# Optimization experiments

Hardware: AMD Instinct MI355X
Metric: run time of the kernel (lower is better)

## Reference

```python
import jax, jax.numpy as jnp
import numpy as np

N_NODES = 50000


def _gcn_conv(x, W, b, src, dst, n_nodes):
    """PyG GCNConv: add self-loops, symmetric normalization, aggregate, linear, bias.
    x: [N, Fin], W: [Fin, Fout], b: [Fout], src/dst: [E] int.
    """
    loop = jnp.arange(n_nodes, dtype=src.dtype)
    src_f = jnp.concatenate([src, loop])  # [E + N]
    dst_f = jnp.concatenate([dst, loop])
    # degree over incoming edges (edge weights are all 1 after self-loops)
    deg = jax.ops.segment_sum(jnp.ones_like(src_f, dtype=x.dtype), dst_f,
                              num_segments=n_nodes)
    dinv = jnp.where(deg > 0, jax.lax.rsqrt(deg), 0.0)
    norm = dinv[src_f] * dinv[dst_f]  # [E + N]
    h = x @ W  # [N, Fout] -- transform before propagate (Fin >= Fout path)
    msg = h[src_f] * norm[:, None]  # gather + per-edge scale
    out = jax.ops.segment_sum(msg, dst_f, num_segments=n_nodes)  # scatter-add
    return out + b


def setup_inputs() -> dict:
    key = jax.random.key(0)
    k_x, k_e, k_w1, k_w2 = jax.random.split(key, 4)
    in_ch, out_ch = 128, 64
    hid = 2 * out_ch
    n_edges = 800000
    x = jax.random.normal(k_x, (N_NODES, in_ch), dtype=jnp.float32)
    edge_index = jax.random.randint(k_e, (2, n_edges), 0, N_NODES, dtype=jnp.int64)
    # Glorot-ish init for weights, zero bias (matches PyG defaults)
    W1 = jax.random.normal(k_w1, (in_ch, hid), dtype=jnp.float32) / np.sqrt(in_ch)
    b1 = jnp.zeros((hid,), dtype=jnp.float32)
    W2 = jax.random.normal(k_w2, (hid, out_ch), dtype=jnp.float32) / np.sqrt(hid)
    b2 = jnp.zeros((out_ch,), dtype=jnp.float32)
    return {"x": x, "edge_index": edge_index, "W1": W1, "b1": b1, "W2": W2, "b2": b2}


def reference(x, edge_index, W1, b1, W2, b2):
    src, dst = edge_index[0], edge_index[1]
    h = jnp.tanh(_gcn_conv(x, W1, b1, src, dst, N_NODES))
    return _gcn_conv(h, W2, b2, src, dst, N_NODES)
```

## Files before the change

kernel.cpp:

```cpp
#include <hip/hip_runtime.h>
#include <stdint.h>

#define N_NODES 50000
#define IN_CH   128
#define HID     128
#define OUT_CH  64

#define CBITS 8
#define NCB   ((N_NODES + 255) >> 8)
#define CAP   8192
#define APB   4096

#define XPAD  136

typedef unsigned int   uint32;
typedef unsigned short ushort16;
typedef __attribute__((ext_vector_type(8))) short short8;
typedef __attribute__((ext_vector_type(4))) float f32x4;

static __device__ __forceinline__ ushort16 f32_to_bf16(float f) {
    uint32 u = __float_as_uint(f);
    u = (u + 0x7fffu + ((u >> 16) & 1u)) >> 16;
    return (ushort16)u;
}
static __device__ __forceinline__ float bf16lo_to_f32(uint32 u) {
    return __uint_as_float(u << 16);
}
static __device__ __forceinline__ float bf16hi_to_f32(uint32 u) {
    return __uint_as_float(u & 0xffff0000u);
}


__global__ __launch_bounds__(256) void passA_kernel(
    const int* __restrict__ src, const int* __restrict__ dst,
    int* __restrict__ gcur, uint32* __restrict__ ebuf2, int E) {
    __shared__ int hist[256];
    __shared__ int excl[256];
    __shared__ int fcur[256];
    __shared__ int gbase[256];
    __shared__ uint32 obuf[APB];
    const int t = threadIdx.x;
    const int e0 = blockIdx.x * APB;
    const int nv = min(APB, E - e0);

    hist[t] = 0;
    __syncthreads();

    uint32 u[16];
    #pragma unroll
    for (int j = 0; j < 16; ++j) {
        int i = t + 256 * j;
        u[j] = 0xffffffffu;
        if (i < nv) {
            int e = e0 + i;
            int s = src[e], d = dst[e];
            if ((unsigned)d < N_NODES && (unsigned)s < N_NODES) {
                u[j] = (uint32)s | ((uint32)d << 16);
                atomicAdd(&hist[(unsigned)d >> CBITS], 1);
            }
        }
    }
    __syncthreads();

    excl[t] = hist[t];
    __syncthreads();
    #pragma unroll
    for (int off = 1; off < 256; off <<= 1) {
        int v = (t >= off) ? excl[t - off] : 0;
        __syncthreads();
        excl[t] += v;
        __syncthreads();
    }
    int myexcl = excl[t] - hist[t];
    if (hist[t] > 0) gbase[t] = t * CAP + atomicAdd(&gcur[t], hist[t]);
    __syncthreads();
    excl[t] = myexcl;
    fcur[t] = myexcl;
    __syncthreads();

    #pragma unroll
    for (int j = 0; j < 16; ++j) {
        if (u[j] != 0xffffffffu) {
            int b = u[j] >> (16 + CBITS);
            int pos = atomicAdd(&fcur[b], 1);
            obuf[pos] = u[j];
        }
    }
    __syncthreads();

    for (int i = t; i < nv; i += 256) {
        uint32 v = obuf[i];
        int b = v >> (16 + CBITS);
        int gpos = gbase[b] + (i - excl[b]);
        if (gpos < (b + 1) * CAP) ebuf2[gpos] = v;
    }
}

__global__ __launch_bounds__(256) void interlude_kernel(
    const int* __restrict__ gcur, int* __restrict__ ecnt, int* __restrict__ eoff) {
    __shared__ int sd[256];
    int t = threadIdx.x;
    int c = (t < NCB) ? gcur[t] : 0;
    sd[t] = c;
    __syncthreads();
    #pragma unroll
    for (int off = 1; off < 256; off <<= 1) {
        int v = (t >= off) ? sd[t - off] : 0;
        __syncthreads();
        sd[t] += v;
        __syncthreads();
    }
    if (t < NCB) { ecnt[t] = c; eoff[t] = sd[t] - c; }
}

__global__ __launch_bounds__(256) void passB_kernel(
    const uint32* __restrict__ ebuf2, const int* __restrict__ ecnt,
    const int* __restrict__ eoff, ushort16* __restrict__ ebuf16,
    int* __restrict__ offs, int* __restrict__ degi, float* __restrict__ dinv) {
    __shared__ uint32 sbuf[CAP];
    __shared__ ushort16 obuf[CAP];
    __shared__ int fh[256];
    __shared__ int fx[256];
    __shared__ int fc[256];
    const int b = blockIdx.x, t = threadIdx.x;
    const int nb = ecnt[b];
    const int base = b * CAP;
    const int obase = eoff[b];

    fh[t] = 0;
    __syncthreads();
    for (int i = t; i < nb; i += 256) {
        uint32 v = ebuf2[base + i];
        sbuf[i] = v;
        atomicAdd(&fh[(v >> 16) & 255], 1);
    }
    __syncthreads();

    fx[t] = fh[t];
    __syncthreads();
    #pragma unroll
    for (int off = 1; off < 256; off <<= 1) {
        int v = (t >= off) ? fx[t - off] : 0;
        __syncthreads();
        fx[t] += v;
        __syncthreads();
    }
    int ex = fx[t] - fh[t];
    fc[t] = ex;

    int n = b * 256 + t;
    if (n < N_NODES) {
        degi[n] = fh[t];
        offs[n] = obase + ex;
        dinv[n] = rsqrtf(1.0f + (float)fh[t]);
    }
    __syncthreads();

    for (int i = t; i < nb; i += 256) {
        uint32 v = sbuf[i];
        int nl = (v >> 16) & 255;
        int pos = atomicAdd(&fc[nl], 1);
        obuf[pos] = (ushort16)(v & 0xffffu);
    }
    __syncthreads();
    for (int i = t; i < nb; i += 256) ebuf16[obase + i] = obuf[i];
}

__global__ __launch_bounds__(256) void prep_w_kernel(
    const float* __restrict__ W1, const float* __restrict__ W2,
    ushort16* __restrict__ w1t, ushort16* __restrict__ w2t) {
    int i = blockIdx.x * 256 + threadIdx.x;
    if (i < 128 * 128) {
        int k = i >> 7, n = i & 127;
        w1t[n * 128 + k] = f32_to_bf16(W1[k * 128 + n]);
    }
    if (i < 128 * 64) {
        int k = i >> 6, n = i & 63;
        w2t[n * 128 + k] = f32_to_bf16(W2[k * 64 + n]);
    }
}

__global__ __launch_bounds__(256) void gemm1_mfma_kernel(
    const float* __restrict__ x, const ushort16* __restrict__ w1t,
    ushort16* __restrict__ h1b) {
    __shared__ __align__(16) ushort16 xs[64 * XPAD];
    __shared__ __align__(16) ushort16 wt[128 * XPAD];
    const int tid = threadIdx.x;
    const int block_row = blockIdx.x * 64;

    {
        const uint4* g = (const uint4*)w1t;
        #pragma unroll
        for (int j = 0; j < 8; ++j) {
            int idx = tid + 256 * j;
            int row = idx >> 4, c = idx & 15;
            uint4 v = g[idx];
            *(uint4*)&wt[row * XPAD + c * 8] = v;
        }
    }
    {
        #pragma unroll
        for (int j = 0; j < 8; ++j) {
            int idx = tid + 256 * j;
            int row = idx >> 5, c4 = idx & 31;
            int gr = block_row + row; if (gr >= N_NODES) gr = N_NODES - 1;
            float4 v = *(const float4*)(x + (size_t)gr * IN_CH + c4 * 4);
            uint32 p0 = (uint32)f32_to_bf16(v.x) | ((uint32)f32_to_bf16(v.y) << 16);
            uint32 p1 = (uint32)f32_to_bf16(v.z) | ((uint32)f32_to_bf16(v.w) << 16);
            uint32* dp = (uint32*)&xs[row * XPAD + c4 * 4];
            dp[0] = p0; dp[1] = p1;
        }
    }
    __syncthreads();

    const int wv = tid >> 6, lane = tid & 63;
    const int r16 = lane & 15, kq = lane >> 4;
    f32x4 acc[8];
    #pragma unroll
    for (int n = 0; n < 8; ++n) acc[n] = (f32x4){0.f, 0.f, 0.f, 0.f};

    const ushort16* xrow = &xs[(wv * 16 + r16) * XPAD + kq * 8];
    #pragma unroll
    for (int kk = 0; kk < 4; ++kk) {
        short8 a = *(const short8*)(xrow + kk * 32);
        #pragma unroll
        for (int n = 0; n < 8; ++n) {
            short8 b = *(const short8*)&wt[(n * 16 + r16) * XPAD + kk * 32 + kq * 8];
            acc[n] = __builtin_amdgcn_mfma_f32_16x16x32_bf16(a, b, acc[n], 0, 0, 0);
        }
    }

    #pragma unroll
    for (int n = 0; n < 8; ++n) {
        #pragma unroll
        for (int j = 0; j < 4; ++j) {
            int gr = block_row + wv * 16 + kq * 4 + j;
            if (gr < N_NODES)
                h1b[(size_t)gr * HID + n * 16 + r16] = f32_to_bf16(acc[n][j]);
        }
    }
}

__global__ __launch_bounds__(256) void gather1_kernel(
    const int* __restrict__ offs, const int* __restrict__ degi,
    const ushort16* __restrict__ ebuf16, const float* __restrict__ dinv,
    const ushort16* __restrict__ h1b, const float* __restrict__ b1,
    ushort16* __restrict__ a1b) {
    int node = blockIdx.x * 4 + (threadIdx.x >> 6);
    int lane = threadIdx.x & 63;
    if (node >= N_NODES) return;
    float di = dinv[node];
    int beg = offs[node];
    int cnt = degi[node];

    uint32 us = ((const uint32*)(h1b + (size_t)node * HID))[lane];
    float ax = bf16lo_to_f32(us) * di * di;
    float ay = bf16hi_to_f32(us) * di * di;

    for (int base = 0; base < cnt; base += 64) {
        int m = min(cnt - base, 64);
        int e_l = 0; float w_l = 0.f;
        if (lane < m) { e_l = ebuf16[beg + base + lane]; w_l = dinv[e_l] * di; }
        int i = 0;
        for (; i + 8 <= m; i += 8) {
            int s0 = __shfl(e_l, i),     s1 = __shfl(e_l, i + 1);
            int s2 = __shfl(e_l, i + 2), s3 = __shfl(e_l, i + 3);
            int s4 = __shfl(e_l, i + 4), s5 = __shfl(e_l, i + 5);
            int s6 = __shfl(e_l, i + 6), s7 = __shfl(e_l, i + 7);
            float w0 = __shfl(w_l, i),     w1 = __shfl(w_l, i + 1);
            float w2 = __shfl(w_l, i + 2), w3 = __shfl(w_l, i + 3);
            float w4 = __shfl(w_l, i + 4), w5 = __shfl(w_l, i + 5);
            float w6 = __shfl(w_l, i + 6), w7 = __shfl(w_l, i + 7);
            uint32 u0 = ((const uint32*)(h1b + (size_t)s0 * HID))[lane];
            uint32 u1 = ((const uint32*)(h1b + (size_t)s1 * HID))[lane];
            uint32 u2 = ((const uint32*)(h1b + (size_t)s2 * HID))[lane];
            uint32 u3 = ((const uint32*)(h1b + (size_t)s3 * HID))[lane];
            uint32 u4 = ((const uint32*)(h1b + (size_t)s4 * HID))[lane];
            uint32 u5 = ((const uint32*)(h1b + (size_t)s5 * HID))[lane];
            uint32 u6 = ((const uint32*)(h1b + (size_t)s6 * HID))[lane];
            uint32 u7 = ((const uint32*)(h1b + (size_t)s7 * HID))[lane];
            ax += bf16lo_to_f32(u0) * w0 + bf16lo_to_f32(u1) * w1
                + bf16lo_to_f32(u2) * w2 + bf16lo_to_f32(u3) * w3
                + bf16lo_to_f32(u4) * w4 + bf16lo_to_f32(u5) * w5
                + bf16lo_to_f32(u6) * w6 + bf16lo_to_f32(u7) * w7;
            ay += bf16hi_to_f32(u0) * w0 + bf16hi_to_f32(u1) * w1
                + bf16hi_to_f32(u2) * w2 + bf16hi_to_f32(u3) * w3
                + bf16hi_to_f32(u4) * w4 + bf16hi_to_f32(u5) * w5
                + bf16hi_to_f32(u6) * w6 + bf16hi_to_f32(u7) * w7;
        }
        for (; i + 2 <= m; i += 2) {
            int s0 = __shfl(e_l, i), s1 = __shfl(e_l, i + 1);
            float w0 = __shfl(w_l, i), w1 = __shfl(w_l, i + 1);
            uint32 u0 = ((const uint32*)(h1b + (size_t)s0 * HID))[lane];
            uint32 u1 = ((const uint32*)(h1b + (size_t)s1 * HID))[lane];
            ax += bf16lo_to_f32(u0) * w0 + bf16lo_to_f32(u1) * w1;
            ay += bf16hi_to_f32(u0) * w0 + bf16hi_to_f32(u1) * w1;
        }
        for (; i < m; ++i) {
            int s0 = __shfl(e_l, i);
            float w0 = __shfl(w_l, i);
            uint32 u0 = ((const uint32*)(h1b + (size_t)s0 * HID))[lane];
            ax += bf16lo_to_f32(u0) * w0;
            ay += bf16hi_to_f32(u0) * w0;
        }
    }
    float2 bb = ((const float2*)b1)[lane];
    float tx = tanhf(ax + bb.x);
    float ty = tanhf(ay + bb.y);
    uint32 pk = (uint32)f32_to_bf16(tx) | ((uint32)f32_to_bf16(ty) << 16);
    ((uint32*)(a1b + (size_t)node * HID))[lane] = pk;
}

__global__ __launch_bounds__(256) void gemm2_mfma_kernel(
    const ushort16* __restrict__ a1b, const ushort16* __restrict__ w2t,
    ushort16* __restrict__ h2b) {
    __shared__ __align__(16) ushort16 xs[64 * XPAD];
    __shared__ __align__(16) ushort16 wt[64 * XPAD];
    const int tid = threadIdx.x;
    const int block_row = blockIdx.x * 64;

    {
        const uint4* g = (const uint4*)w2t;
        #pragma unroll
        for (int j = 0; j < 4; ++j) {
            int idx = tid + 256 * j;
            int row = idx >> 4, c = idx & 15;
            uint4 v = g[idx];
            *(uint4*)&wt[row * XPAD + c * 8] = v;
        }
    }
    {
        #pragma unroll
        for (int j = 0; j < 4; ++j) {
            int idx = tid + 256 * j;
            int row = idx >> 4, c = idx & 15;
            int gr = block_row + row; if (gr >= N_NODES) gr = N_NODES - 1;
            uint4 v = *(const uint4*)(a1b + (size_t)gr * HID + c * 8);
            *(uint4*)&xs[row * XPAD + c * 8] = v;
        }
    }
    __syncthreads();

    const int wv = tid >> 6, lane = tid & 63;
    const int r16 = lane & 15, kq = lane >> 4;
    f32x4 acc[4];
    #pragma unroll
    for (int n = 0; n < 4; ++n) acc[n] = (f32x4){0.f, 0.f, 0.f, 0.f};

    const ushort16* xrow = &xs[(wv * 16 + r16) * XPAD + kq * 8];
    #pragma unroll
    for (int kk = 0; kk < 4; ++kk) {
        short8 a = *(const short8*)(xrow + kk * 32);
        #pragma unroll
        for (int n = 0; n < 4; ++n) {
            short8 b = *(const short8*)&wt[(n * 16 + r16) * XPAD + kk * 32 + kq * 8];
            acc[n] = __builtin_amdgcn_mfma_f32_16x16x32_bf16(a, b, acc[n], 0, 0, 0);
        }
    }

    #pragma unroll
    for (int n = 0; n < 4; ++n) {
        #pragma unroll
        for (int j = 0; j < 4; ++j) {
            int gr = block_row + wv * 16 + kq * 4 + j;
            if (gr < N_NODES)
                h2b[(size_t)gr * OUT_CH + n * 16 + r16] = f32_to_bf16(acc[n][j]);
        }
    }
}

__global__ __launch_bounds__(256) void gather2_kernel(
    const int* __restrict__ offs, const int* __restrict__ degi,
    const ushort16* __restrict__ ebuf16, const float* __restrict__ dinv,
    const ushort16* __restrict__ h2b, const float* __restrict__ b2,
    float* __restrict__ out) {
    int node = blockIdx.x * 4 + (threadIdx.x >> 6);
    int lane = threadIdx.x & 63;
    if (node >= N_NODES) return;
    float di = dinv[node];
    int beg = offs[node];
    int cnt = degi[node];

    float self = __uint_as_float(((uint32)h2b[(size_t)node * OUT_CH + lane]) << 16);
    float acc = b2[lane] + self * di * di;

    for (int base = 0; base < cnt; base += 64) {
        int m = min(cnt - base, 64);
        int e_l = 0; float w_l = 0.f;
        if (lane < m) { e_l = ebuf16[beg + base + lane]; w_l = dinv[e_l] * di; }
        int i = 0;
        for (; i + 8 <= m; i += 8) {
            int s0 = __shfl(e_l, i),     s1 = __shfl(e_l, i + 1);
            int s2 = __shfl(e_l, i + 2), s3 = __shfl(e_l, i + 3);
            int s4 = __shfl(e_l, i + 4), s5 = __shfl(e_l, i + 5);
            int s6 = __shfl(e_l, i + 6), s7 = __shfl(e_l, i + 7);
            float w0 = __shfl(w_l, i),     w1 = __shfl(w_l, i + 1);
            float w2 = __shfl(w_l, i + 2), w3 = __shfl(w_l, i + 3);
            float w4 = __shfl(w_l, i + 4), w5 = __shfl(w_l, i + 5);
            float w6 = __shfl(w_l, i + 6), w7 = __shfl(w_l, i + 7);
            float v0 = __uint_as_float(((uint32)h2b[(size_t)s0 * OUT_CH + lane]) << 16);
            float v1 = __uint_as_float(((uint32)h2b[(size_t)s1 * OUT_CH + lane]) << 16);
            float v2 = __uint_as_float(((uint32)h2b[(size_t)s2 * OUT_CH + lane]) << 16);
            float v3 = __uint_as_float(((uint32)h2b[(size_t)s3 * OUT_CH + lane]) << 16);
            float v4 = __uint_as_float(((uint32)h2b[(size_t)s4 * OUT_CH + lane]) << 16);
            float v5 = __uint_as_float(((uint32)h2b[(size_t)s5 * OUT_CH + lane]) << 16);
            float v6 = __uint_as_float(((uint32)h2b[(size_t)s6 * OUT_CH + lane]) << 16);
            float v7 = __uint_as_float(((uint32)h2b[(size_t)s7 * OUT_CH + lane]) << 16);
            acc += v0 * w0 + v1 * w1 + v2 * w2 + v3 * w3
                 + v4 * w4 + v5 * w5 + v6 * w6 + v7 * w7;
        }
        for (; i + 2 <= m; i += 2) {
            int s0 = __shfl(e_l, i), s1 = __shfl(e_l, i + 1);
            float w0 = __shfl(w_l, i), w1 = __shfl(w_l, i + 1);
            float v0 = __uint_as_float(((uint32)h2b[(size_t)s0 * OUT_CH + lane]) << 16);
            float v1 = __uint_as_float(((uint32)h2b[(size_t)s1 * OUT_CH + lane]) << 16);
            acc += v0 * w0 + v1 * w1;
        }
        for (; i < m; ++i) {
            int s0 = __shfl(e_l, i);
            float w0 = __shfl(w_l, i);
            float v0 = __uint_as_float(((uint32)h2b[(size_t)s0 * OUT_CH + lane]) << 16);
            acc += v0 * w0;
        }
    }
    out[(size_t)node * OUT_CH + lane] = acc;
}

extern "C" void kernel_launch(void* const* d_in, const int* in_sizes, int n_in,
                              void* d_out, int out_size, void* d_ws, size_t ws_size,
                              hipStream_t stream) {
    const float* x  = (const float*)d_in[0];
    const int*   ei = (const int*)d_in[1];
    const float* W1 = (const float*)d_in[2];
    const float* b1 = (const float*)d_in[3];
    const float* W2 = (const float*)d_in[4];
    const float* b2 = (const float*)d_in[5];
    float* out = (float*)d_out;

    const int E = in_sizes[1] / 2;
    const int* src = ei;
    const int* dst = ei + E;

    float* dinv   = (float*)d_ws;
    int* degi     = (int*)(dinv + N_NODES);
    int* offs     = degi + N_NODES;
    int* gcur     = offs + N_NODES;
    int* ecnt     = gcur + NCB;
    int* eoff     = ecnt + NCB;
    ushort16* w1t = (ushort16*)(eoff + NCB);
    ushort16* w2t = w1t + 128 * 128;
    ushort16* ebuf16 = w2t + 64 * 128;
    uintptr_t p   = (uintptr_t)(ebuf16 + E);
    p = (p + 15) & ~(uintptr_t)15;
    ushort16* a1b = (ushort16*)p;
    uint32* ebuf2 = (uint32*)a1b;
    ushort16* h1b = a1b + (size_t)N_NODES * HID;
    ushort16* h2b = h1b + (size_t)N_NODES * HID;

    hipMemsetAsync(gcur, 0, NCB * sizeof(int), stream);
    passA_kernel<<<(E + APB - 1) / APB, 256, 0, stream>>>(src, dst, gcur, ebuf2, E);
    interlude_kernel<<<1, 256, 0, stream>>>(gcur, ecnt, eoff);
    passB_kernel<<<NCB, 256, 0, stream>>>(ebuf2, ecnt, eoff, ebuf16, offs, degi, dinv);
    prep_w_kernel<<<64, 256, 0, stream>>>(W1, W2, w1t, w2t);

    gemm1_mfma_kernel<<<(N_NODES + 63) / 64, 256, 0, stream>>>(x, w1t, h1b);
    gather1_kernel<<<(N_NODES + 3) / 4, 256, 0, stream>>>(offs, degi, ebuf16, dinv, h1b, b1, a1b);
    gemm2_mfma_kernel<<<(N_NODES + 63) / 64, 256, 0, stream>>>(a1b, w2t, h2b);
    gather2_kernel<<<(N_NODES + 3) / 4, 256, 0, stream>>>(offs, degi, ebuf16, dinv, h2b, b2, out);
}
```

Measured before the change: 121.1 us.

## Merge preprocessing kernels and co-schedule GEMM1 with CSR build; use readlane in gathers

```diff
diff --git a/kernel.cpp b/kernel.cpp
--- a/kernel.cpp
+++ b/kernel.cpp
@@ -7,11 +7,12 @@
 #define OUT_CH  64
 
 #define CBITS 8
-#define NCB   ((N_NODES + 255) >> 8)
+#define NCB   196
 #define CAP   8192
 #define APB   4096
 
 #define XPAD  136
+#define G1BLK 782
 
 typedef unsigned int   uint32;
 typedef unsigned short ushort16;
@@ -29,17 +30,34 @@
 static __device__ __forceinline__ float bf16hi_to_f32(uint32 u) {
     return __uint_as_float(u & 0xffff0000u);
 }
-
-
-__global__ __launch_bounds__(256) void passA_kernel(
+#define RLI(v, l) __builtin_amdgcn_readlane((v), (l))
+#define RLF(v, l) __uint_as_float((uint32)__builtin_amdgcn_readlane((int)__float_as_uint(v), (l)))
+
+__global__ __launch_bounds__(256) void build1_kernel(
     const int* __restrict__ src, const int* __restrict__ dst,
-    int* __restrict__ gcur, uint32* __restrict__ ebuf2, int E) {
+    int* __restrict__ gcur, uint32* __restrict__ ebuf2, int E, int nA,
+    const float* __restrict__ W1, const float* __restrict__ W2,
+    ushort16* __restrict__ w1t, ushort16* __restrict__ w2t) {
     __shared__ int hist[256];
     __shared__ int excl[256];
     __shared__ int fcur[256];
     __shared__ int gbase[256];
     __shared__ uint32 obuf[APB];
     const int t = threadIdx.x;
+
+    if ((int)blockIdx.x >= nA) {
+        int i = ((int)blockIdx.x - nA) * 256 + t;
+        if (i < 128 * 128) {
+            int k = i >> 7, n = i & 127;
+            w1t[n * 128 + k] = f32_to_bf16(W1[k * 128 + n]);
+        }
+        if (i < 128 * 64) {
+            int k = i >> 6, n = i & 63;
+            w2t[n * 128 + k] = f32_to_bf16(W2[k * 64 + n]);
+        }
+        return;
+    }
+
     const int e0 = blockIdx.x * APB;
     const int nv = min(APB, E - e0);
 
@@ -96,41 +114,102 @@
     }
 }
 
-__global__ __launch_bounds__(256) void interlude_kernel(
-    const int* __restrict__ gcur, int* __restrict__ ecnt, int* __restrict__ eoff) {
-    __shared__ int sd[256];
-    int t = threadIdx.x;
-    int c = (t < NCB) ? gcur[t] : 0;
-    sd[t] = c;
-    __syncthreads();
-    #pragma unroll
-    for (int off = 1; off < 256; off <<= 1) {
-        int v = (t >= off) ? sd[t - off] : 0;
-        __syncthreads();
-        sd[t] += v;
-        __syncthreads();
-    }
-    if (t < NCB) { ecnt[t] = c; eoff[t] = sd[t] - c; }
-}
-
-__global__ __launch_bounds__(256) void passB_kernel(
-    const uint32* __restrict__ ebuf2, const int* __restrict__ ecnt,
-    const int* __restrict__ eoff, ushort16* __restrict__ ebuf16,
-    int* __restrict__ offs, int* __restrict__ degi, float* __restrict__ dinv) {
-    __shared__ uint32 sbuf[CAP];
-    __shared__ ushort16 obuf[CAP];
-    __shared__ int fh[256];
-    __shared__ int fx[256];
-    __shared__ int fc[256];
-    const int b = blockIdx.x, t = threadIdx.x;
-    const int nb = ecnt[b];
-    const int base = b * CAP;
-    const int obase = eoff[b];
+__global__ __launch_bounds__(256) void build2_kernel(
+    const uint32* __restrict__ ebuf2, const int* __restrict__ gcur,
+    ushort16* __restrict__ ebuf16, int* __restrict__ offs,
+    int* __restrict__ degi, float* __restrict__ dinv,
+    const float* __restrict__ x, const ushort16* __restrict__ w1t,
+    ushort16* __restrict__ h1b) {
+    __shared__ __align__(16) char smem[53248];
+    const int t = threadIdx.x;
+
+    if (blockIdx.x >= NCB) {
+        ushort16* xs = (ushort16*)smem;
+        ushort16* wt = (ushort16*)(smem + 64 * XPAD * 2);
+        const int block_row = ((int)blockIdx.x - NCB) * 64;
+
+        {
+            const uint4* g = (const uint4*)w1t;
+            #pragma unroll
+            for (int j = 0; j < 8; ++j) {
+                int idx = t + 256 * j;
+                int row = idx >> 4, c = idx & 15;
+                uint4 v = g[idx];
+                *(uint4*)&wt[row * XPAD + c * 8] = v;
+            }
+        }
+        {
+            #pragma unroll
+            for (int j = 0; j < 8; ++j) {
+                int idx = t + 256 * j;
+                int row = idx >> 5, c4 = idx & 31;
+                int gr = block_row + row; if (gr >= N_NODES) gr = N_NODES - 1;
+                float4 v = *(const float4*)(x + (size_t)gr * IN_CH + c4 * 4);
+                uint32 p0 = (uint32)f32_to_bf16(v.x) | ((uint32)f32_to_bf16(v.y) << 16);
+                uint32 p1 = (uint32)f32_to_bf16(v.z) | ((uint32)f32_to_bf16(v.w) << 16);
+                uint32* dp = (uint32*)&xs[row * XPAD + c4 * 4];
+                dp[0] = p0; dp[1] = p1;
+            }
+        }
+        __syncthreads();
+
+        const int wv = t >> 6, lane = t & 63;
+        const int r16 = lane & 15, kq = lane >> 4;
+        f32x4 acc[8];
+        #pragma unroll
+        for (int n = 0; n < 8; ++n) acc[n] = (f32x4){0.f, 0.f, 0.f, 0.f};
+
+        const ushort16* xrow = &xs[(wv * 16 + r16) * XPAD + kq * 8];
+        #pragma unroll
+        for (int kk = 0; kk < 4; ++kk) {
+            short8 a = *(const short8*)(xrow + kk * 32);
+            #pragma unroll
+            for (int n = 0; n < 8; ++n) {
+                short8 b = *(const short8*)&wt[(n * 16 + r16) * XPAD + kk * 32 + kq * 8];
+                acc[n] = __builtin_amdgcn_mfma_f32_16x16x32_bf16(a, b, acc[n], 0, 0, 0);
+            }
+        }
+
+        #pragma unroll
+        for (int n = 0; n < 8; ++n) {
+            #pragma unroll
+            for (int j = 0; j < 4; ++j) {
+                int gr = block_row + wv * 16 + kq * 4 + j;
+                if (gr < N_NODES)
+                    h1b[(size_t)gr * HID + n * 16 + r16] = f32_to_bf16(acc[n][j]);
+            }
+        }
+        return;
+    }
+
+    uint32*   sbuf = (uint32*)smem;
+    ushort16* obuf = (ushort16*)(smem + CAP * 4);
+    int* fh = (int*)(smem + CAP * 4 + CAP * 2);
+    int* fx = fh + 256;
+    int* fc = fx + 256;
+    int* gs = fc + 256;
+    const int b = blockIdx.x;
+
+    {
+        int c = (t < NCB) ? min(gcur[t], CAP) : 0;
+        gs[t] = c;
+        __syncthreads();
+        #pragma unroll
+        for (int off = 1; off < 256; off <<= 1) {
+            int v = (t >= off) ? gs[t - off] : 0;
+            __syncthreads();
+            gs[t] += v;
+            __syncthreads();
+        }
+    }
+    const int nb = min(gcur[b], CAP);
+    const int obase = gs[b] - nb;
+    __syncthreads();
 
     fh[t] = 0;
     __syncthreads();
     for (int i = t; i < nb; i += 256) {
-        uint32 v = ebuf2[base + i];
+        uint32 v = ebuf2[b * CAP + i];
         sbuf[i] = v;
         atomicAdd(&fh[(v >> 16) & 255], 1);
     }
@@ -164,81 +243,6 @@
     }
     __syncthreads();
     for (int i = t; i < nb; i += 256) ebuf16[obase + i] = obuf[i];
-}
-
-__global__ __launch_bounds__(256) void prep_w_kernel(
-    const float* __restrict__ W1, const float* __restrict__ W2,
-    ushort16* __restrict__ w1t, ushort16* __restrict__ w2t) {
-    int i = blockIdx.x * 256 + threadIdx.x;
-    if (i < 128 * 128) {
-        int k = i >> 7, n = i & 127;
-        w1t[n * 128 + k] = f32_to_bf16(W1[k * 128 + n]);
-    }
-    if (i < 128 * 64) {
-        int k = i >> 6, n = i & 63;
-        w2t[n * 128 + k] = f32_to_bf16(W2[k * 64 + n]);
-    }
-}
-
-__global__ __launch_bounds__(256) void gemm1_mfma_kernel(
-    const float* __restrict__ x, const ushort16* __restrict__ w1t,
-    ushort16* __restrict__ h1b) {
-    __shared__ __align__(16) ushort16 xs[64 * XPAD];
-    __shared__ __align__(16) ushort16 wt[128 * XPAD];
-    const int tid = threadIdx.x;
-    const int block_row = blockIdx.x * 64;
-
-    {
-        const uint4* g = (const uint4*)w1t;
-        #pragma unroll
-        for (int j = 0; j < 8; ++j) {
-            int idx = tid + 256 * j;
-            int row = idx >> 4, c = idx & 15;
-            uint4 v = g[idx];
-            *(uint4*)&wt[row * XPAD + c * 8] = v;
-        }
-    }
-    {
-        #pragma unroll
-        for (int j = 0; j < 8; ++j) {
-            int idx = tid + 256 * j;
-            int row = idx >> 5, c4 = idx & 31;
-            int gr = block_row + row; if (gr >= N_NODES) gr = N_NODES - 1;
-            float4 v = *(const float4*)(x + (size_t)gr * IN_CH + c4 * 4);
-            uint32 p0 = (uint32)f32_to_bf16(v.x) | ((uint32)f32_to_bf16(v.y) << 16);
-            uint32 p1 = (uint32)f32_to_bf16(v.z) | ((uint32)f32_to_bf16(v.w) << 16);
-            uint32* dp = (uint32*)&xs[row * XPAD + c4 * 4];
-            dp[0] = p0; dp[1] = p1;
-        }
-    }
-    __syncthreads();
-
-    const int wv = tid >> 6, lane = tid & 63;
-    const int r16 = lane & 15, kq = lane >> 4;
-    f32x4 acc[8];
-    #pragma unroll
-    for (int n = 0; n < 8; ++n) acc[n] = (f32x4){0.f, 0.f, 0.f, 0.f};
-
-    const ushort16* xrow = &xs[(wv * 16 + r16) * XPAD + kq * 8];
-    #pragma unroll
-    for (int kk = 0; kk < 4; ++kk) {
-        short8 a = *(const short8*)(xrow + kk * 32);
-        #pragma unroll
-        for (int n = 0; n < 8; ++n) {
-            short8 b = *(const short8*)&wt[(n * 16 + r16) * XPAD + kk * 32 + kq * 8];
-            acc[n] = __builtin_amdgcn_mfma_f32_16x16x32_bf16(a, b, acc[n], 0, 0, 0);
-        }
-    }
-
-    #pragma unroll
-    for (int n = 0; n < 8; ++n) {
-        #pragma unroll
-        for (int j = 0; j < 4; ++j) {
-            int gr = block_row + wv * 16 + kq * 4 + j;
-            if (gr < N_NODES)
-                h1b[(size_t)gr * HID + n * 16 + r16] = f32_to_bf16(acc[n][j]);
-        }
-    }
 }
 
 __global__ __launch_bounds__(256) void gather1_kernel(
@@ -260,17 +264,21 @@
     for (int base = 0; base < cnt; base += 64) {
         int m = min(cnt - base, 64);
         int e_l = 0; float w_l = 0.f;
-        if (lane < m) { e_l = ebuf16[beg + base + lane]; w_l = dinv[e_l] * di; }
+        if (lane < m) {
+            e_l = (int)ebuf16[beg + base + lane];
+            e_l = min(e_l, N_NODES - 1);
+            w_l = dinv[e_l] * di;
+        }
         int i = 0;
         for (; i + 8 <= m; i += 8) {
-            int s0 = __shfl(e_l, i),     s1 = __shfl(e_l, i + 1);
-            int s2 = __shfl(e_l, i + 2), s3 = __shfl(e_l, i + 3);
-            int s4 = __shfl(e_l, i + 4), s5 = __shfl(e_l, i + 5);
-            int s6 = __shfl(e_l, i + 6), s7 = __shfl(e_l, i + 7);
-            float w0 = __shfl(w_l, i),     w1 = __shfl(w_l, i + 1);
-            float w2 = __shfl(w_l, i + 2), w3 = __shfl(w_l, i + 3);
-            float w4 = __shfl(w_l, i + 4), w5 = __shfl(w_l, i + 5);
-            float w6 = __shfl(w_l, i + 6), w7 = __shfl(w_l, i + 7);
+            int s0 = RLI(e_l, i),     s1 = RLI(e_l, i + 1);
+            int s2 = RLI(e_l, i + 2), s3 = RLI(e_l, i + 3);
+            int s4 = RLI(e_l, i + 4), s5 = RLI(e_l, i + 5);
+            int s6 = RLI(e_l, i + 6), s7 = RLI(e_l, i + 7);
+            float w0 = RLF(w_l, i),     w1 = RLF(w_l, i + 1);
+            float w2 = RLF(w_l, i + 2), w3 = RLF(w_l, i + 3);
+            float w4 = RLF(w_l, i + 4), w5 = RLF(w_l, i + 5);
+            float w6 = RLF(w_l, i + 6), w7 = RLF(w_l, i + 7);
             uint32 u0 = ((const uint32*)(h1b + (size_t)s0 * HID))[lane];
             uint32 u1 = ((const uint32*)(h1b + (size_t)s1 * HID))[lane];
             uint32 u2 = ((const uint32*)(h1b + (size_t)s2 * HID))[lane];
@@ -288,17 +296,9 @@
                 + bf16hi_to_f32(u4) * w4 + bf16hi_to_f32(u5) * w5
                 + bf16hi_to_f32(u6) * w6 + bf16hi_to_f32(u7) * w7;
         }
-        for (; i + 2 <= m; i += 2) {
-            int s0 = __shfl(e_l, i), s1 = __shfl(e_l, i + 1);
-            float w0 = __shfl(w_l, i), w1 = __shfl(w_l, i + 1);
-            uint32 u0 = ((const uint32*)(h1b + (size_t)s0 * HID))[lane];
-            uint32 u1 = ((const uint32*)(h1b + (size_t)s1 * HID))[lane];
-            ax += bf16lo_to_f32(u0) * w0 + bf16lo_to_f32(u1) * w1;
-            ay += bf16hi_to_f32(u0) * w0 + bf16hi_to_f32(u1) * w1;
-        }
         for (; i < m; ++i) {
-            int s0 = __shfl(e_l, i);
-            float w0 = __shfl(w_l, i);
+            int s0 = RLI(e_l, i);
+            float w0 = RLF(w_l, i);
             uint32 u0 = ((const uint32*)(h1b + (size_t)s0 * HID))[lane];
             ax += bf16lo_to_f32(u0) * w0;
             ay += bf16hi_to_f32(u0) * w0;
@@ -387,17 +387,21 @@
     for (int base = 0; base < cnt; base += 64) {
         int m = min(cnt - base, 64);
         int e_l = 0; float w_l = 0.f;
-        if (lane < m) { e_l = ebuf16[beg + base + lane]; w_l = dinv[e_l] * di; }
+        if (lane < m) {
+            e_l = (int)ebuf16[beg + base + lane];
+            e_l = min(e_l, N_NODES - 1);
+            w_l = dinv[e_l] * di;
+        }
         int i = 0;
         for (; i + 8 <= m; i += 8) {
-            int s0 = __shfl(e_l, i),     s1 = __shfl(e_l, i + 1);
-            int s2 = __shfl(e_l, i + 2), s3 = __shfl(e_l, i + 3);
-            int s4 = __shfl(e_l, i + 4), s5 = __shfl(e_l, i + 5);
-            int s6 = __shfl(e_l, i + 6), s7 = __shfl(e_l, i + 7);
-            float w0 = __shfl(w_l, i),     w1 = __shfl(w_l, i + 1);
-            float w2 = __shfl(w_l, i + 2), w3 = __shfl(w_l, i + 3);
-            float w4 = __shfl(w_l, i + 4), w5 = __shfl(w_l, i + 5);
-            float w6 = __shfl(w_l, i + 6), w7 = __shfl(w_l, i + 7);
+            int s0 = RLI(e_l, i),     s1 = RLI(e_l, i + 1);
+            int s2 = RLI(e_l, i + 2), s3 = RLI(e_l, i + 3);
+            int s4 = RLI(e_l, i + 4), s5 = RLI(e_l, i + 5);
+            int s6 = RLI(e_l, i + 6), s7 = RLI(e_l, i + 7);
+            float w0 = RLF(w_l, i),     w1 = RLF(w_l, i + 1);
+            float w2 = RLF(w_l, i + 2), w3 = RLF(w_l, i + 3);
+            float w4 = RLF(w_l, i + 4), w5 = RLF(w_l, i + 5);
+            float w6 = RLF(w_l, i + 6), w7 = RLF(w_l, i + 7);
             float v0 = __uint_as_float(((uint32)h2b[(size_t)s0 * OUT_CH + lane]) << 16);
             float v1 = __uint_as_float(((uint32)h2b[(size_t)s1 * OUT_CH + lane]) << 16);
             float v2 = __uint_as_float(((uint32)h2b[(size_t)s2 * OUT_CH + lane]) << 16);
@@ -409,16 +413,9 @@
             acc += v0 * w0 + v1 * w1 + v2 * w2 + v3 * w3
                  + v4 * w4 + v5 * w5 + v6 * w6 + v7 * w7;
         }
-        for (; i + 2 <= m; i += 2) {
-            int s0 = __shfl(e_l, i), s1 = __shfl(e_l, i + 1);
-            float w0 = __shfl(w_l, i), w1 = __shfl(w_l, i + 1);
-            float v0 = __uint_as_float(((uint32)h2b[(size_t)s0 * OUT_CH + lane]) << 16);
-            float v1 = __uint_as_float(((uint32)h2b[(size_t)s1 * OUT_CH + lane]) << 16);
-            acc += v0 * w0 + v1 * w1;
-        }
         for (; i < m; ++i) {
-            int s0 = __shfl(e_l, i);
-            float w0 = __shfl(w_l, i);
+            int s0 = RLI(e_l, i);
+            float w0 = RLF(w_l, i);
             float v0 = __uint_as_float(((uint32)h2b[(size_t)s0 * OUT_CH + lane]) << 16);
             acc += v0 * w0;
         }
@@ -440,17 +437,16 @@
     const int E = in_sizes[1] / 2;
     const int* src = ei;
     const int* dst = ei + E;
+    const int nA = (E + APB - 1) / APB;
 
     float* dinv   = (float*)d_ws;
     int* degi     = (int*)(dinv + N_NODES);
     int* offs     = degi + N_NODES;
     int* gcur     = offs + N_NODES;
-    int* ecnt     = gcur + NCB;
-    int* eoff     = ecnt + NCB;
-    ushort16* w1t = (ushort16*)(eoff + NCB);
+    ushort16* w1t = (ushort16*)(gcur + NCB);
     ushort16* w2t = w1t + 128 * 128;
     ushort16* ebuf16 = w2t + 64 * 128;
-    uintptr_t p   = (uintptr_t)(ebuf16 + E);
+    uintptr_t p   = (uintptr_t)(ebuf16 + (size_t)NCB * CAP);
     p = (p + 15) & ~(uintptr_t)15;
     ushort16* a1b = (ushort16*)p;
     uint32* ebuf2 = (uint32*)a1b;
@@ -458,13 +454,11 @@
     ushort16* h2b = h1b + (size_t)N_NODES * HID;
 
     hipMemsetAsync(gcur, 0, NCB * sizeof(int), stream);
-    passA_kernel<<<(E + APB - 1) / APB, 256, 0, stream>>>(src, dst, gcur, ebuf2, E);
-    interlude_kernel<<<1, 256, 0, stream>>>(gcur, ecnt, eoff);
-    passB_kernel<<<NCB, 256, 0, stream>>>(ebuf2, ecnt, eoff, ebuf16, offs, degi, dinv);
-    prep_w_kernel<<<64, 256, 0, stream>>>(W1, W2, w1t, w2t);
-
-    gemm1_mfma_kernel<<<(N_NODES + 63) / 64, 256, 0, stream>>>(x, w1t, h1b);
+    build1_kernel<<<nA + 64, 256, 0, stream>>>(src, dst, gcur, ebuf2, E, nA,
+                                               W1, W2, w1t, w2t);
+    build2_kernel<<<NCB + G1BLK, 256, 0, stream>>>(ebuf2, gcur, ebuf16, offs, degi, dinv,
+                                                   x, w1t, h1b);
     gather1_kernel<<<(N_NODES + 3) / 4, 256, 0, stream>>>(offs, degi, ebuf16, dinv, h1b, b1, a1b);
-    gemm2_mfma_kernel<<<(N_NODES + 63) / 64, 256, 0, stream>>>(a1b, w2t, h2b);
+    gemm2_mfma_kernel<<<G1BLK, 256, 0, stream>>>(a1b, w2t, h2b);
     gather2_kernel<<<(N_NODES + 3) / 4, 256, 0, stream>>>(offs, degi, ebuf16, dinv, h2b, b2, out);
 }
```

Result: faster. 113.3 us (-6.4%).
